# Kernel tuning notes

Measured on AMD Instinct MI355X. Metric: run time of the kernel, lower is better.

The kernel has to match this reference:

```python
import jax, jax.numpy as jnp
import numpy as np

NUM_TREES = 4096
TOTAL_NODES = 1048576
D = 256


def _make_tree_sizes():
    # ragged, strictly positive sizes summing exactly to TOTAL_NODES
    rng = np.random.default_rng(0)
    cuts = np.sort(rng.choice(TOTAL_NODES - 1, NUM_TREES - 1, replace=False) + 1)
    bounds = np.concatenate([[0], cuts, [TOTAL_NODES]])
    return jnp.asarray(np.diff(bounds), dtype=jnp.int64)


def setup_inputs() -> dict:
    key = jax.random.key(0)
    embeddings = jax.random.normal(key, (TOTAL_NODES, D), dtype=jnp.float32)
    tree_sizes = _make_tree_sizes()
    return {"embeddings": embeddings, "tree_sizes": tree_sizes}


def reference(embeddings, tree_sizes):
    num_trees = tree_sizes.shape[0]
    total = embeddings.shape[0]
    # groups[j] = tree index of node j (contiguous segments)
    groups = jnp.repeat(jnp.arange(num_trees, dtype=jnp.int32), tree_sizes,
                        total_repeat_length=total)
    # segmented max over dim 0 -> [num_trees, D]
    return jax.ops.segment_max(embeddings, groups, num_segments=num_trees)
```

## Files before the change

kernel.cpp:

```cpp
#include <hip/hip_runtime.h>
#include <math.h>

#define NUM_TREES 4096
#define TOTAL_NODES 1048576
#define DCOL 256
#define DPW 64
#define CHUNK 256
#define NC_MAX 8192

static __device__ __forceinline__ unsigned enc(float f) {
    unsigned b = __float_as_uint(f);
    return (b & 0x80000000u) ? ~b : (b | 0x80000000u);
}
static __device__ __forceinline__ float dec(unsigned u) {
    return (u & 0x80000000u) ? __uint_as_float(u ^ 0x80000000u)
                             : __uint_as_float(~u);
}
#define ENC_NEG_INF 0x007FFFFFu

static __device__ __forceinline__ float4 f4max(float4 a, float4 b) {
    float4 r;
    r.x = fmaxf(a.x, b.x);
    r.y = fmaxf(a.y, b.y);
    r.z = fmaxf(a.z, b.z);
    r.w = fmaxf(a.w, b.w);
    return r;
}

__global__ void TreeAgg_prep(const void* __restrict__ sizes_raw,
                             int* __restrict__ row_off,
                             int* __restrict__ chunk_off) {
    __shared__ int s_row[256];
    __shared__ int s_chk[256];
    __shared__ int s_is64;
    const int t = threadIdx.x;
    const int base = t * 16;
    const int* s32 = (const int*)sizes_raw;

    int ls[16];
    int rsum = 0;
    #pragma unroll
    for (int i = 0; i < 16; ++i) {
        ls[i] = s32[base + i];
        rsum += ls[i];
    }
    s_row[t] = rsum;
    __syncthreads();
    if (t == 0) {
        long long tot = 0;
        for (int i = 0; i < 256; ++i) tot += (long long)s_row[i];
        s_is64 = (tot != (long long)TOTAL_NODES) ? 1 : 0;
    }
    __syncthreads();
    if (s_is64) {
        const long long* s64 = (const long long*)sizes_raw;
        #pragma unroll
        for (int i = 0; i < 16; ++i) ls[i] = (int)s64[base + i];
    }

    int rs = 0, cs = 0;
    #pragma unroll
    for (int i = 0; i < 16; ++i) {
        rs += ls[i];
        cs += (ls[i] + CHUNK - 1) / CHUNK;
    }
    s_row[t] = rs;
    s_chk[t] = cs;
    __syncthreads();
    if (t == 0) {
        int ra = 0, ca = 0;
        for (int i = 0; i < 256; ++i) {
            int r = s_row[i], c = s_chk[i];
            s_row[i] = ra; s_chk[i] = ca;
            ra += r; ca += c;
        }
        row_off[NUM_TREES] = ra;
        chunk_off[NUM_TREES] = ca;
    }
    __syncthreads();
    int ro = s_row[t], co = s_chk[t];
    #pragma unroll
    for (int i = 0; i < 16; ++i) {
        row_off[base + i] = ro;
        chunk_off[base + i] = co;
        ro += ls[i];
        co += (ls[i] + CHUNK - 1) / CHUNK;
    }
}

__global__ void TreeAgg_init(unsigned* __restrict__ out_u) {
    const int i = blockIdx.x * blockDim.x + threadIdx.x;
    uint4 v = make_uint4(ENC_NEG_INF, ENC_NEG_INF, ENC_NEG_INF, ENC_NEG_INF);
    ((uint4*)out_u)[i] = v;
}

__global__ void TreeAgg_partial(const float* __restrict__ emb,
                                const int* __restrict__ row_off,
                                const int* __restrict__ chunk_off,
                                unsigned* __restrict__ out_u) {
    const int wid  = (blockIdx.x * blockDim.x + threadIdx.x) >> 6;
    const int lane = threadIdx.x & 63;
    const int NC = chunk_off[NUM_TREES];
    if (wid >= NC) return;

    int lo = 0, hi = NUM_TREES;
    while (hi - lo > 1) {
        int mid = (lo + hi) >> 1;
        if (chunk_off[mid] <= wid) lo = mid; else hi = mid;
    }
    const int t  = lo;
    const int k  = wid - chunk_off[t];
    int r0 = row_off[t] + k * CHUNK;
    int r1 = min(r0 + CHUNK, row_off[t + 1]);
    r1 = min(r1, TOTAL_NODES);
    r0 = max(0, min(r0, r1));
    if (r0 >= r1) return;

    const float4* __restrict__ src = (const float4*)emb;
    const float NEG = -INFINITY;
    float4 acc = make_float4(NEG, NEG, NEG, NEG);

    long idx = (long)r0 * DPW + lane;
    int r = r0;
    for (; r + 4 <= r1; r += 4, idx += 4 * DPW) {
        float4 a = src[idx];
        float4 b = src[idx + DPW];
        float4 c = src[idx + 2 * DPW];
        float4 d = src[idx + 3 * DPW];
        acc = f4max(acc, f4max(f4max(a, b), f4max(c, d)));
    }
    for (; r < r1; ++r, idx += DPW) {
        acc = f4max(acc, src[idx]);
    }

    unsigned* dst = out_u + (long)t * DCOL + lane * 4;
    atomicMax(dst + 0, enc(acc.x));
    atomicMax(dst + 1, enc(acc.y));
    atomicMax(dst + 2, enc(acc.z));
    atomicMax(dst + 3, enc(acc.w));
}

__global__ void TreeAgg_decode(unsigned* __restrict__ out_u) {
    const int i = blockIdx.x * blockDim.x + threadIdx.x;
    uint4 v = ((uint4*)out_u)[i];
    float4 f;
    f.x = dec(v.x); f.y = dec(v.y); f.z = dec(v.z); f.w = dec(v.w);
    ((float4*)out_u)[i] = f;
}

extern "C" void kernel_launch(void* const* d_in, const int* in_sizes, int n_in,
                              void* d_out, int out_size, void* d_ws, size_t ws_size,
                              hipStream_t stream) {
    const float* emb   = (const float*)d_in[0];
    const void*  sizes = d_in[1];
    unsigned*    out_u = (unsigned*)d_out;

    char* ws = (char*)d_ws;
    int* row_off   = (int*)(ws);
    int* chunk_off = (int*)(ws + 20480);

    TreeAgg_prep<<<1, 256, 0, stream>>>(sizes, row_off, chunk_off);

    TreeAgg_init<<<1024, 256, 0, stream>>>(out_u);

    const int p1_blocks = (NC_MAX * 64) / 256;
    TreeAgg_partial<<<p1_blocks, 256, 0, stream>>>(emb, row_off, chunk_off, out_u);

    TreeAgg_decode<<<1024, 256, 0, stream>>>(out_u);
}
```

Baseline: 241.5 us.

## Split rows into fixed slices per wave and fuse prep, init and decode

```diff
diff --git a/kernel.cpp b/kernel.cpp
--- a/kernel.cpp
+++ b/kernel.cpp
@@ -5,18 +5,8 @@
 #define TOTAL_NODES 1048576
 #define DCOL 256
 #define DPW 64
-#define CHUNK 256
-#define NC_MAX 8192
-
-static __device__ __forceinline__ unsigned enc(float f) {
-    unsigned b = __float_as_uint(f);
-    return (b & 0x80000000u) ? ~b : (b | 0x80000000u);
-}
-static __device__ __forceinline__ float dec(unsigned u) {
-    return (u & 0x80000000u) ? __uint_as_float(u ^ 0x80000000u)
-                             : __uint_as_float(~u);
-}
-#define ENC_NEG_INF 0x007FFFFFu
+#define SLICE 128
+#define NWAVES 8192
 
 static __device__ __forceinline__ float4 f4max(float4 a, float4 b) {
     float4 r;
@@ -27,125 +17,108 @@
     return r;
 }
 
-__global__ void TreeAgg_prep(const void* __restrict__ sizes_raw,
-                             int* __restrict__ row_off,
-                             int* __restrict__ chunk_off) {
-    __shared__ int s_row[256];
-    __shared__ int s_chk[256];
-    __shared__ int s_is64;
-    const int t = threadIdx.x;
-    const int base = t * 16;
-    const int* s32 = (const int*)sizes_raw;
-
-    int ls[16];
-    int rsum = 0;
-    #pragma unroll
-    for (int i = 0; i < 16; ++i) {
-        ls[i] = s32[base + i];
-        rsum += ls[i];
-    }
-    s_row[t] = rsum;
-    __syncthreads();
-    if (t == 0) {
-        long long tot = 0;
-        for (int i = 0; i < 256; ++i) tot += (long long)s_row[i];
-        s_is64 = (tot != (long long)TOTAL_NODES) ? 1 : 0;
-    }
-    __syncthreads();
-    if (s_is64) {
-        const long long* s64 = (const long long*)sizes_raw;
-        #pragma unroll
-        for (int i = 0; i < 16; ++i) ls[i] = (int)s64[base + i];
-    }
-
-    int rs = 0, cs = 0;
-    #pragma unroll
-    for (int i = 0; i < 16; ++i) {
-        rs += ls[i];
-        cs += (ls[i] + CHUNK - 1) / CHUNK;
-    }
-    s_row[t] = rs;
-    s_chk[t] = cs;
-    __syncthreads();
-    if (t == 0) {
-        int ra = 0, ca = 0;
-        for (int i = 0; i < 256; ++i) {
-            int r = s_row[i], c = s_chk[i];
-            s_row[i] = ra; s_chk[i] = ca;
-            ra += r; ca += c;
-        }
-        row_off[NUM_TREES] = ra;
-        chunk_off[NUM_TREES] = ca;
-    }
-    __syncthreads();
-    int ro = s_row[t], co = s_chk[t];
-    #pragma unroll
-    for (int i = 0; i < 16; ++i) {
-        row_off[base + i] = ro;
-        chunk_off[base + i] = co;
-        ro += ls[i];
-        co += (ls[i] + CHUNK - 1) / CHUNK;
+static __device__ __forceinline__ void atomicFmax(float* addr, float val) {
+    unsigned* u = (unsigned*)addr;
+    unsigned old = *u;
+    while (__uint_as_float(old) < val) {
+        unsigned assumed = old;
+        old = atomicCAS(u, assumed, __float_as_uint(val));
+        if (old == assumed) break;
     }
 }
 
-__global__ void TreeAgg_init(unsigned* __restrict__ out_u) {
-    const int i = blockIdx.x * blockDim.x + threadIdx.x;
-    uint4 v = make_uint4(ENC_NEG_INF, ENC_NEG_INF, ENC_NEG_INF, ENC_NEG_INF);
-    ((uint4*)out_u)[i] = v;
+__global__ void TreeAgg_prep_init(const void* __restrict__ sizes_raw,
+                                  int* __restrict__ row_off,
+                                  float* __restrict__ out) {
+    if (blockIdx.x == 0) {
+        __shared__ int s_row[256];
+        __shared__ int s_is64;
+        const int t = threadIdx.x;
+        const int base = t * 16;
+        const int* s32 = (const int*)sizes_raw;
+
+        int ls[16];
+        int rsum = 0;
+        #pragma unroll
+        for (int i = 0; i < 16; ++i) { ls[i] = s32[base + i]; rsum += ls[i]; }
+        s_row[t] = rsum;
+        __syncthreads();
+        if (t == 0) {
+            long long tot = 0;
+            for (int i = 0; i < 256; ++i) tot += (long long)s_row[i];
+            s_is64 = (tot != (long long)TOTAL_NODES) ? 1 : 0;
+        }
+        __syncthreads();
+        if (s_is64) {
+            const long long* s64 = (const long long*)sizes_raw;
+            #pragma unroll
+            for (int i = 0; i < 16; ++i) ls[i] = (int)s64[base + i];
+            int rs = 0;
+            #pragma unroll
+            for (int i = 0; i < 16; ++i) rs += ls[i];
+            s_row[t] = rs;
+            __syncthreads();
+        }
+        if (t == 0) {
+            int ra = 0;
+            for (int i = 0; i < 256; ++i) { int r = s_row[i]; s_row[i] = ra; ra += r; }
+            row_off[NUM_TREES] = ra;
+        }
+        __syncthreads();
+        int ro = s_row[t];
+        #pragma unroll
+        for (int i = 0; i < 16; ++i) { row_off[base + i] = ro; ro += ls[i]; }
+    } else {
+        const int i = (blockIdx.x - 1) * blockDim.x + threadIdx.x;
+        const float NEG = -INFINITY;
+        ((float4*)out)[i] = make_float4(NEG, NEG, NEG, NEG);
+    }
 }
 
-__global__ void TreeAgg_partial(const float* __restrict__ emb,
-                                const int* __restrict__ row_off,
-                                const int* __restrict__ chunk_off,
-                                unsigned* __restrict__ out_u) {
+__global__ __launch_bounds__(256, 8)
+void TreeAgg_main(const float* __restrict__ emb,
+                  const int* __restrict__ row_off,
+                  float* __restrict__ out) {
     const int wid  = (blockIdx.x * blockDim.x + threadIdx.x) >> 6;
     const int lane = threadIdx.x & 63;
-    const int NC = chunk_off[NUM_TREES];
-    if (wid >= NC) return;
+
+    int a = wid * SLICE;
+    const int bend = a + SLICE;
 
     int lo = 0, hi = NUM_TREES;
     while (hi - lo > 1) {
         int mid = (lo + hi) >> 1;
-        if (chunk_off[mid] <= wid) lo = mid; else hi = mid;
+        if (row_off[mid] <= a) lo = mid; else hi = mid;
     }
-    const int t  = lo;
-    const int k  = wid - chunk_off[t];
-    int r0 = row_off[t] + k * CHUNK;
-    int r1 = min(r0 + CHUNK, row_off[t + 1]);
-    r1 = min(r1, TOTAL_NODES);
-    r0 = max(0, min(r0, r1));
-    if (r0 >= r1) return;
+    int t = lo;
 
     const float4* __restrict__ src = (const float4*)emb;
     const float NEG = -INFINITY;
-    float4 acc = make_float4(NEG, NEG, NEG, NEG);
+    long idx = (long)a * DPW + lane;
 
-    long idx = (long)r0 * DPW + lane;
-    int r = r0;
-    for (; r + 4 <= r1; r += 4, idx += 4 * DPW) {
-        float4 a = src[idx];
-        float4 b = src[idx + DPW];
-        float4 c = src[idx + 2 * DPW];
-        float4 d = src[idx + 3 * DPW];
-        acc = f4max(acc, f4max(f4max(a, b), f4max(c, d)));
+    while (a < bend) {
+        int b = min(bend, row_off[t + 1]);
+        if (b <= a) break;
+        float4 acc = make_float4(NEG, NEG, NEG, NEG);
+        int r = a;
+        for (; r + 4 <= b; r += 4, idx += 4 * DPW) {
+            float4 x = src[idx];
+            float4 y = src[idx + DPW];
+            float4 z = src[idx + 2 * DPW];
+            float4 w = src[idx + 3 * DPW];
+            acc = f4max(acc, f4max(f4max(x, y), f4max(z, w)));
+        }
+        for (; r < b; ++r, idx += DPW) {
+            acc = f4max(acc, src[idx]);
+        }
+        float* dst = out + (long)t * DCOL + lane * 4;
+        atomicFmax(dst + 0, acc.x);
+        atomicFmax(dst + 1, acc.y);
+        atomicFmax(dst + 2, acc.z);
+        atomicFmax(dst + 3, acc.w);
+        a = b;
+        ++t;
     }
-    for (; r < r1; ++r, idx += DPW) {
-        acc = f4max(acc, src[idx]);
-    }
-
-    unsigned* dst = out_u + (long)t * DCOL + lane * 4;
-    atomicMax(dst + 0, enc(acc.x));
-    atomicMax(dst + 1, enc(acc.y));
-    atomicMax(dst + 2, enc(acc.z));
-    atomicMax(dst + 3, enc(acc.w));
-}
-
-__global__ void TreeAgg_decode(unsigned* __restrict__ out_u) {
-    const int i = blockIdx.x * blockDim.x + threadIdx.x;
-    uint4 v = ((uint4*)out_u)[i];
-    float4 f;
-    f.x = dec(v.x); f.y = dec(v.y); f.z = dec(v.z); f.w = dec(v.w);
-    ((float4*)out_u)[i] = f;
 }
 
 extern "C" void kernel_launch(void* const* d_in, const int* in_sizes, int n_in,
@@ -153,18 +126,11 @@
                               hipStream_t stream) {
     const float* emb   = (const float*)d_in[0];
     const void*  sizes = d_in[1];
-    unsigned*    out_u = (unsigned*)d_out;
+    float*       out   = (float*)d_out;
 
-    char* ws = (char*)d_ws;
-    int* row_off   = (int*)(ws);
-    int* chunk_off = (int*)(ws + 20480);
+    int* row_off = (int*)d_ws;
 
-    TreeAgg_prep<<<1, 256, 0, stream>>>(sizes, row_off, chunk_off);
+    TreeAgg_prep_init<<<1025, 256, 0, stream>>>(sizes, row_off, out);
 
-    TreeAgg_init<<<1024, 256, 0, stream>>>(out_u);
-
-    const int p1_blocks = (NC_MAX * 64) / 256;
-    TreeAgg_partial<<<p1_blocks, 256, 0, stream>>>(emb, row_off, chunk_off, out_u);
-
-    TreeAgg_decode<<<1024, 256, 0, stream>>>(out_u);
+    TreeAgg_main<<<NWAVES * 64 / 256, 256, 0, stream>>>(emb, row_off, out);
 }
```

New measurement: 238.7 us. About the same (-1.2%).
